# Optimization experiments

Hardware: AMD Instinct MI355X
Metric: run time of the kernel (lower is better)

The kernel has to match this reference:

```python
import jax, jax.numpy as jnp
import numpy as np

C64 = jnp.complex64


def _rx(theta):
    # RX(t) = [[cos(t/2), -i sin(t/2)], [-i sin(t/2), cos(t/2)]]; theta scalar or [B]
    h = 0.5 * theta
    c = jnp.cos(h).astype(C64)
    s = (-1j * jnp.sin(h)).astype(C64)
    return jnp.stack([jnp.stack([c, s], -1), jnp.stack([s, c], -1)], -2)


def _ry(theta):
    h = 0.5 * theta
    c = jnp.cos(h).astype(C64)
    s = jnp.sin(h).astype(C64)
    return jnp.stack([jnp.stack([c, -s], -1), jnp.stack([s, c], -1)], -2)


def _rz(theta):
    h = 0.5 * theta
    em = jnp.exp(-1j * h).astype(C64)
    ep = jnp.exp(1j * h).astype(C64)
    z = jnp.zeros_like(em)
    return jnp.stack([jnp.stack([em, z], -1), jnp.stack([z, ep], -1)], -2)


def _apply_1q(state, U, q):
    # state: [B, 2^Q] complex; wire 0 is the most significant bit.
    B = state.shape[0]
    s = state.reshape(B, 2 ** q, 2, -1)
    if U.ndim == 3:  # batched gate [B,2,2]
        s = jnp.einsum('bij,bajc->baic', U, s)
    else:  # shared gate [2,2]
        s = jnp.einsum('ij,bajc->baic', U, s)
    return s.reshape(B, -1)


def _cnot_adj(state, q):
    # CNOT with control q, target q+1 (adjacent wires)
    B = state.shape[0]
    s = state.reshape(B, 2 ** q, 2, 2, -1)
    s = s.at[:, :, 1].set(s[:, :, 1, ::-1])
    return s.reshape(B, -1)


def _pqc(context, W, b, pqc_params):
    Q = W.shape[0]
    L = pqc_params.shape[0]
    angles = jnp.pi * jnp.tanh(context @ W.T + b)  # [B, Q]
    B = angles.shape[0]
    state = jnp.zeros((B, 2 ** Q), C64).at[:, 0].set(1.0)
    # data-encoding RX layer (batch-dependent angles)
    for q in range(Q):
        state = _apply_1q(state, _rx(angles[:, q]), q)
    # variational layers
    for l in range(L):
        for q in range(Q):
            state = _apply_1q(state, _rx(pqc_params[l, q, 0]), q)
            state = _apply_1q(state, _ry(pqc_params[l, q, 1]), q)
            state = _apply_1q(state, _rz(pqc_params[l, q, 2]), q)
        for q in range(Q - 1):
            state = _cnot_adj(state, q)
    # <Z_q> expectation for every wire
    probs = state.real ** 2 + state.imag ** 2  # [B, 2^Q]
    p = probs.reshape((B,) + (2,) * Q)
    z = [p.sum(tuple(i + 1 for i in range(Q) if i != q)) for q in range(Q)]  # each [B,2]
    z = jnp.stack(z, -1)  # [B, 2, Q] -> wait: stack of [B,2] on -1 -> [B,2,Q]
    return z[:, 0, :] - z[:, 1, :]  # [B, Q]


def setup_inputs() -> dict:
    key = jax.random.key(0)
    k0, k1, k2, k3 = jax.random.split(key, 4)
    B, D, Q, L = 512, 256, 16, 4
    context = jax.random.normal(k0, (B, D), jnp.float32)
    W = jax.random.normal(k1, (Q, D), jnp.float32) / np.float32(np.sqrt(D))
    b = 0.01 * jax.random.normal(k2, (Q,), jnp.float32)
    pqc_params = 0.01 * jax.random.normal(k3, (L, Q, 3), jnp.float32)
    return {"context": context, "W": W, "b": b, "pqc_params": pqc_params}


def reference(context, W, b, pqc_params):
    return _pqc(context, W, b, pqc_params)
```

## Files before the change

kernel.cpp:

```cpp
#include <hip/hip_runtime.h>
#include <math.h>

#define NQ   16
#define NTH  256
#define NB   512

typedef float2 c32;

__device__ __forceinline__ c32 cmul(c32 a, c32 b) {
    return make_float2(a.x*b.x - a.y*b.y, a.x*b.y + a.y*b.x);
}
__device__ __forceinline__ c32 cfma_(c32 a, c32 b, c32 acc) {
    acc.x = fmaf(a.x, b.x, fmaf(-a.y, b.y, acc.x));
    acc.y = fmaf(a.x, b.y, fmaf( a.y, b.x, acc.y));
    return acc;
}
__device__ __forceinline__ c32 cfmaConjA(c32 a, c32 b, c32 acc) {
    acc.x = fmaf(a.x, b.x, fmaf( a.y, b.y, acc.x));
    acc.y = fmaf(a.x, b.y, fmaf(-a.y, b.x, acc.y));
    return acc;
}
__device__ __forceinline__ c32 cmulConjA(c32 a, c32 b) {
    return cfmaConjA(a, b, make_float2(0.f, 0.f));
}
__device__ __forceinline__ c32 cadd(c32 a, c32 b){ return make_float2(a.x+b.x, a.y+b.y); }


__global__ __launch_bounds__(NTH, 2)
void pqc_mps_kernel(const float* __restrict__ ctx,
                    const float* __restrict__ Wm,
                    const float* __restrict__ bias,
                    const float* __restrict__ params,
                    float* __restrict__ out)
{
    __shared__ c32 Ac[14][272];
    __shared__ c32 A0c[16];
    __shared__ c32 A15v[32];
    __shared__ c32 Renv[15][144];
    __shared__ c32 Ssto[15][144];
    __shared__ c32 TR[272];
    __shared__ c32 TL[272];
    __shared__ c32 Lbuf[144];
    __shared__ c32 Ug[256];
    __shared__ c32 wv[64];
    __shared__ float angles[NQ];

    const int b = blockIdx.x;
    const int t = threadIdx.x;

    {
        const int q = t >> 4, g = t & 15;
        const float* crow = ctx + b * 256;
        const float* wrow = Wm + q * 256;
        float s = 0.f;
        #pragma unroll
        for (int j = 0; j < 16; ++j)
            s += crow[g + 16*j] * wrow[g + 16*j];
        #pragma unroll
        for (int m = 8; m; m >>= 1) s += __shfl_xor(s, m);
        if (g == 0) angles[q] = 3.14159265358979323846f * tanhf(s + bias[q]);
    }
    if (t < 64) {
        const float a  = params[t*3 + 0];
        const float bb = params[t*3 + 1];
        const float c  = params[t*3 + 2];
        const float ha = 0.5f*a, hb = 0.5f*bb, hc = 0.5f*c;
        const float ca = cosf(ha), sa = sinf(ha);
        const float cb = cosf(hb), sb = sinf(hb);
        const float cz = cosf(hc), sz = sinf(hc);
        const c32 m00 = make_float2( cb*ca,  sb*sa);
        const c32 m01 = make_float2(-sb*ca, -cb*sa);
        const c32 m10 = make_float2( sb*ca, -cb*sa);
        const c32 m11 = make_float2( cb*ca, -sb*sa);
        const c32 e0 = make_float2(cz, -sz);
        const c32 e1 = make_float2(cz,  sz);
        Ug[t*4 + 0] = cmul(e0, m00);
        Ug[t*4 + 1] = cmul(e0, m01);
        Ug[t*4 + 2] = cmul(e1, m10);
        Ug[t*4 + 3] = cmul(e1, m11);
    }
    __syncthreads();

    if (t < 64) {
        const int q = t >> 2, k = (t>>1)&1, i = t&1;
        const float h = 0.5f * angles[q];
        const float ch = cosf(h), sh = sinf(h);
        const int r0 = (i ^ k) << 1;
        const c32 u0 = Ug[(q<<2) + r0];
        const c32 u1 = Ug[(q<<2) + r0 + 1];
        wv[t] = make_float2(u0.x*ch + u1.y*sh, u0.y*ch - u1.x*sh);
    }
    __syncthreads();

    {
        const int r = t & 7, i = (t>>3)&1, a = t>>4;
        const int m0 = r&1, m1 = (r>>1)&1, m2 = r>>2;
        const int k0 = a&1, k1 = (a>>1)&1, k2 = (a>>2)&1, k3 = a>>3;
        #pragma unroll
        for (int q = 1; q <= 14; ++q) {
            const c32 u3 = Ug[((48+q)<<2) + ((i ^k3)<<1) + m2];
            const c32 u2 = Ug[((32+q)<<2) + ((m2^k2)<<1) + m1];
            const c32 u1 = Ug[((16+q)<<2) + ((m1^k1)<<1) + m0];
            const c32 ww = wv[(q<<2) + (k0<<1) + m0];
            Ac[q-1][a*17 + i*8 + r] = cmul(cmul(u3, u2), cmul(u1, ww));
        }
        if (t < 16) {
            const c32 u3 = Ug[(48<<2) + (i <<1) + m2];
            const c32 u2 = Ug[(32<<2) + (m2<<1) + m1];
            const c32 u1 = Ug[(16<<2) + (m1<<1) + m0];
            A0c[t] = cmul(cmul(u3, u2), cmul(u1, wv[m0]));
        }
        if (t >= 64 && t < 96) {
            const int idx = t - 64, aa = idx >> 1, ii = idx & 1;
            const int K0 = aa&1, K1 = (aa>>1)&1, K2 = (aa>>2)&1, K3 = aa>>3;
            c32 y1[2], y2[2];
            #pragma unroll
            for (int j1 = 0; j1 < 2; ++j1) {
                const int rr = (j1 ^ K1) << 1;
                y1[j1] = cfma_(Ug[((16+15)<<2)+rr], wv[60 + (K0<<1)],
                         cmul (Ug[((16+15)<<2)+rr+1], wv[60 + (K0<<1) + 1]));
            }
            #pragma unroll
            for (int j2 = 0; j2 < 2; ++j2) {
                const int rr = (j2 ^ K2) << 1;
                y2[j2] = cfma_(Ug[((32+15)<<2)+rr], y1[0],
                         cmul (Ug[((32+15)<<2)+rr+1], y1[1]));
            }
            const int rr = (ii ^ K3) << 1;
            A15v[(aa<<1)+ii] = cfma_(Ug[((48+15)<<2)+rr], y2[0],
                               cmul (Ug[((48+15)<<2)+rr+1], y2[1]));
        }
    }
    __syncthreads();

    if (t < 128) {
        const int m = t>>6, bl = (t>>3)&7, bp = t&7;
        c32 acc = cmulConjA(A15v[((m<<3)+bl)<<1],       A15v[((m<<3)+bp)<<1]);
        acc     = cfmaConjA(A15v[(((m<<3)+bl)<<1) + 1], A15v[(((m<<3)+bp)<<1) + 1], acc);
        Renv[14][m*72 + bl*9 + bp] = acc;
    } else {
        const int u = t-128, i = u>>6, bl = (u>>3)&7, bp = u&7;
        const c32 s = cmulConjA(A0c[(i<<3)+bl], A0c[(i<<3)+bp]);
        Ssto[0][i*72 + bl*9 + bp] = s;
        Lbuf   [i*72 + bl*9 + bp] = s;
    }
    __syncthreads();

    for (int s = 1; s <= 14; ++s) {
        const c32* Ap = Ac[14 - s];
        const c32* Rn = Renv[15 - s];
        const c32* As = Ac[s - 1];

        {
            const int bb = t>>4, i = (t>>3)&1, gp = t&7;
            const int m = bb>>3, al = bb&7;
            c32 tr = make_float2(0.f,0.f), tl = make_float2(0.f,0.f);
            #pragma unroll
            for (int g = 0; g < 8; ++g) {
                tr = cfmaConjA(Ap[bb*17 + i*8 + g], Rn[i*72 + g*9 + gp], tr);
                tl = cfma_(Lbuf[m*72 + al*9 + g], As[(m*8+g)*17 + i*8 + gp], tl);
            }
            TR[bb*17 + i*8 + gp] = tr;
            TL[bb*17 + i*8 + gp] = tl;
        }
        __syncthreads();

        if (t < 128) {
            const int m = t>>6, bl = (t>>3)&7, bp = t&7;
            const c32* trow = &TR[(m*8+bl)*17];
            const c32* arow = &Ap[(m*8+bp)*17];
            c32 r0 = make_float2(0.f,0.f), r1 = make_float2(0.f,0.f);
            #pragma unroll
            for (int ig = 0; ig < 16; ig += 2) {
                r0 = cfma_(trow[ig],   arow[ig],   r0);
                r1 = cfma_(trow[ig+1], arow[ig+1], r1);
            }
            Renv[14-s][m*72 + bl*9 + bp] = cadd(r0, r1);
        } else {
            const int u = t-128, i = u>>6, bl = (u>>3)&7, bp = u&7;
            c32 s0 = make_float2(0.f,0.f), s1 = make_float2(0.f,0.f);
            #pragma unroll
            for (int a = 0; a < 16; a += 2) {
                s0 = cfmaConjA(As[ a   *17 + i*8 + bl], TL[ a   *17 + i*8 + bp], s0);
                s1 = cfmaConjA(As[(a+1)*17 + i*8 + bl], TL[(a+1)*17 + i*8 + bp], s1);
            }
            const c32 sv = cadd(s0, s1);
            Ssto[s][i*72 + bl*9 + bp] = sv;
            Lbuf   [i*72 + bl*9 + bp] = sv;
        }
        __syncthreads();
    }

    {
        const int q = t >> 4, g = t & 15;
        float val = 0.f;
        if (q < 15) {
            const int i = g>>3, bl = g&7;
            const float sign = i ? -1.f : 1.f;
            const c32* Sq = &Ssto[q][i*72 + bl*9];
            const c32* Rq = &Renv[q][i*72 + bl*9];
            #pragma unroll
            for (int j = 0; j < 8; ++j)
                val += sign * (Sq[j].x*Rq[j].x - Sq[j].y*Rq[j].y);
        } else {
            const int m = g>>3, al = g&7;
            const c32 a0 = A15v[((m*8+al)<<1) + 0];
            const c32 a1 = A15v[((m*8+al)<<1) + 1];
            #pragma unroll
            for (int j = 0; j < 8; ++j) {
                c32 d = cmulConjA(a0, A15v[((m*8+j)<<1) + 0]);
                const c32 d1 = cmulConjA(a1, A15v[((m*8+j)<<1) + 1]);
                d.x -= d1.x; d.y -= d1.y;
                const c32 Lv = Lbuf[m*72 + al*9 + j];
                val += Lv.x*d.x - Lv.y*d.y;
            }
        }
        #pragma unroll
        for (int mm = 8; mm; mm >>= 1) val += __shfl_xor(val, mm);
        if (g == 0) out[b*NQ + q] = val;
    }
}

extern "C" void kernel_launch(void* const* d_in, const int* in_sizes, int n_in,
                              void* d_out, int out_size, void* d_ws, size_t ws_size,
                              hipStream_t stream) {
    const float* ctx    = (const float*)d_in[0];
    const float* Wm     = (const float*)d_in[1];
    const float* bias   = (const float*)d_in[2];
    const float* params = (const float*)d_in[3];
    float* out = (float*)d_out;
    (void)in_sizes; (void)n_in; (void)out_size; (void)d_ws; (void)ws_size;
    pqc_mps_kernel<<<NB, NTH, 0, stream>>>(ctx, Wm, bias, params, out);
}
```

Baseline: 79.42 us.

## Split MPS environment sweeps into independent wavefronts with Hermitian-symmetric outputs

The block shrinks to 128 threads. The right-environment sweep runs on wavefront 0 and the left-environment sweep on wavefront 1, each independently, which removes the per-step block-wide __syncthreads barriers. Each thread computes a 2x2 register tile of the intermediate contraction. Only the upper triangle of the Hermitian environment matrices is computed, and the conjugate is mirrored into the other half. The angle dot product now uses float4 loads. The cost is less parallelism per block and a reliance on wavefront-synchronous execution within each 64-lane wave for the shared-memory handoffs between sub-steps.

New measurement: 78.95 us. About the same (-0.6%).

```diff
diff --git a/kernel.cpp b/kernel.cpp
--- a/kernel.cpp
+++ b/kernel.cpp
@@ -2,8 +2,9 @@
 #include <math.h>
 
 #define NQ   16
-#define NTH  256
 #define NB   512
+#define NTH  128
+#define PI_F 3.14159265358979323846f
 
 typedef float2 c32;
 
@@ -23,23 +24,24 @@
 __device__ __forceinline__ c32 cmulConjA(c32 a, c32 b) {
     return cfmaConjA(a, b, make_float2(0.f, 0.f));
 }
+__device__ __forceinline__ c32 conjc(c32 a){ return make_float2(a.x, -a.y); }
 __device__ __forceinline__ c32 cadd(c32 a, c32 b){ return make_float2(a.x+b.x, a.y+b.y); }
 
 
-__global__ __launch_bounds__(NTH, 2)
+__global__ __launch_bounds__(NTH)
 void pqc_mps_kernel(const float* __restrict__ ctx,
                     const float* __restrict__ Wm,
                     const float* __restrict__ bias,
                     const float* __restrict__ params,
                     float* __restrict__ out)
 {
-    __shared__ c32 Ac[14][272];
+    __shared__ c32 Ac[14*272];
     __shared__ c32 A0c[16];
     __shared__ c32 A15v[32];
-    __shared__ c32 Renv[15][144];
-    __shared__ c32 Ssto[15][144];
-    __shared__ c32 TR[272];
-    __shared__ c32 TL[272];
+    __shared__ c32 Renv[15*144];
+    __shared__ c32 Ssto[15*144];
+    __shared__ c32 TRb[272];
+    __shared__ c32 TLT[272];
     __shared__ c32 Lbuf[144];
     __shared__ c32 Ug[256];
     __shared__ c32 wv[64];
@@ -47,18 +49,20 @@
 
     const int b = blockIdx.x;
     const int t = threadIdx.x;
+    const int lane = t & 63;
 
     {
-        const int q = t >> 4, g = t & 15;
-        const float* crow = ctx + b * 256;
-        const float* wrow = Wm + q * 256;
+        const int q = t >> 3, g = t & 7;
+        const float4* c4 = (const float4*)(ctx + (size_t)b * 256);
+        const float4* w4 = (const float4*)(Wm  + (size_t)q * 256);
         float s = 0.f;
         #pragma unroll
-        for (int j = 0; j < 16; ++j)
-            s += crow[g + 16*j] * wrow[g + 16*j];
-        #pragma unroll
-        for (int m = 8; m; m >>= 1) s += __shfl_xor(s, m);
-        if (g == 0) angles[q] = 3.14159265358979323846f * tanhf(s + bias[q]);
+        for (int j = 0; j < 8; ++j) {
+            const float4 x = c4[g + 8*j], y = w4[g + 8*j];
+            s = fmaf(x.x,y.x, fmaf(x.y,y.y, fmaf(x.z,y.z, fmaf(x.w,y.w, s))));
+        }
+        s += __shfl_xor(s, 4); s += __shfl_xor(s, 2); s += __shfl_xor(s, 1);
+        if (g == 0) angles[q] = PI_F * tanhf(s + bias[q]);
     }
     if (t < 64) {
         const float a  = params[t*3 + 0];
@@ -93,18 +97,23 @@
     __syncthreads();
 
     {
-        const int r = t & 7, i = (t>>3)&1, a = t>>4;
-        const int m0 = r&1, m1 = (r>>1)&1, m2 = r>>2;
-        const int k0 = a&1, k1 = (a>>1)&1, k2 = (a>>2)&1, k3 = a>>3;
-        #pragma unroll
         for (int q = 1; q <= 14; ++q) {
-            const c32 u3 = Ug[((48+q)<<2) + ((i ^k3)<<1) + m2];
-            const c32 u2 = Ug[((32+q)<<2) + ((m2^k2)<<1) + m1];
-            const c32 u1 = Ug[((16+q)<<2) + ((m1^k1)<<1) + m0];
-            const c32 ww = wv[(q<<2) + (k0<<1) + m0];
-            Ac[q-1][a*17 + i*8 + r] = cmul(cmul(u3, u2), cmul(u1, ww));
+            #pragma unroll
+            for (int h = 0; h < 2; ++h) {
+                const int idx = t + 128*h;
+                const int r = idx & 7, i = (idx>>3)&1, a = idx>>4;
+                const int m0 = r&1, m1 = (r>>1)&1, m2 = r>>2;
+                const int k0 = a&1, k1 = (a>>1)&1, k2 = (a>>2)&1, k3 = a>>3;
+                const c32 u3 = Ug[((48+q)<<2) + ((i ^k3)<<1) + m2];
+                const c32 u2 = Ug[((32+q)<<2) + ((m2^k2)<<1) + m1];
+                const c32 u1 = Ug[((16+q)<<2) + ((m1^k1)<<1) + m0];
+                const c32 ww = wv[(q<<2) + (k0<<1) + m0];
+                Ac[(q-1)*272 + a*17 + i*8 + r] = cmul(cmul(u3, u2), cmul(u1, ww));
+            }
         }
         if (t < 16) {
+            const int i = t>>3, r = t&7;
+            const int m0 = r&1, m1 = (r>>1)&1, m2 = r>>2;
             const c32 u3 = Ug[(48<<2) + (i <<1) + m2];
             const c32 u2 = Ug[(32<<2) + (m2<<1) + m1];
             const c32 u1 = Ug[(16<<2) + (m1<<1) + m0];
@@ -133,91 +142,201 @@
     }
     __syncthreads();
 
-    if (t < 128) {
-        const int m = t>>6, bl = (t>>3)&7, bp = t&7;
-        c32 acc = cmulConjA(A15v[((m<<3)+bl)<<1],       A15v[((m<<3)+bp)<<1]);
-        acc     = cfmaConjA(A15v[(((m<<3)+bl)<<1) + 1], A15v[(((m<<3)+bp)<<1) + 1], acc);
-        Renv[14][m*72 + bl*9 + bp] = acc;
+    int blJ = 0, bpJ, mJ;
+    {
+        const int r = (lane < 36) ? lane : lane - 36;
+        mJ = (lane >= 36) ? 1 : 0;
+        while ((blJ+1)*(blJ+2)/2 <= r) ++blJ;
+        bpJ = r - blJ*(blJ+1)/2;
+    }
+    const bool has2 = (lane < 8);
+
+    if (t < 64) {
+        const int bbp = lane>>3, iS = (lane>>2)&1, gpp = lane&3;
+        const int bb0 = 2*bbp, bb1 = bb0+1, gq0 = 2*gpp, gq1 = gq0+1;
+
+        {
+            c32 acc = make_float2(0.f,0.f);
+            #pragma unroll
+            for (int i = 0; i < 2; ++i)
+                acc = cfmaConjA(A15v[(mJ*8+blJ)*2+i], A15v[(mJ*8+bpJ)*2+i], acc);
+            Renv[14*144 + mJ*72 + blJ*9 + bpJ] = acc;
+            if (blJ != bpJ) Renv[14*144 + mJ*72 + bpJ*9 + blJ] = conjc(acc);
+            if (has2) {
+                c32 a2 = make_float2(0.f,0.f);
+                #pragma unroll
+                for (int i = 0; i < 2; ++i)
+                    a2 = cfmaConjA(A15v[(8+7)*2+i], A15v[(8+lane)*2+i], a2);
+                Renv[14*144 + 72 + 7*9 + lane] = a2;
+                if (lane != 7) Renv[14*144 + 72 + lane*9 + 7] = conjc(a2);
+            }
+        }
+        for (int s = 1; s <= 14; ++s) {
+            const c32* Ap = Ac + (14-s)*272;
+            const c32* Rn = Renv + (15-s)*144;
+            c32*       Ro = Renv + (14-s)*144;
+            c32 aA[8], aB[8], rA[8], rB[8];
+            #pragma unroll
+            for (int g = 0; g < 8; ++g) {
+                aA[g] = Ap[bb0*17 + iS*8 + g];
+                aB[g] = Ap[bb1*17 + iS*8 + g];
+                rA[g] = Rn[iS*72 + gq0*9 + g];
+                rB[g] = Rn[iS*72 + gq1*9 + g];
+            }
+            c32 t00=make_float2(0.f,0.f), t01=t00, t10=t00, t11=t00;
+            #pragma unroll
+            for (int g = 0; g < 8; ++g) {
+                t00 = cfma_(aA[g], rA[g], t00); t01 = cfma_(aA[g], rB[g], t01);
+                t10 = cfma_(aB[g], rA[g], t10); t11 = cfma_(aB[g], rB[g], t11);
+            }
+            TRb[bb0*17 + iS*8 + gq0] = conjc(t00);
+            TRb[bb0*17 + iS*8 + gq1] = conjc(t01);
+            TRb[bb1*17 + iS*8 + gq0] = conjc(t10);
+            TRb[bb1*17 + iS*8 + gq1] = conjc(t11);
+            {
+                const c32* tr = TRb + (mJ*8+blJ)*17;
+                const c32* ap = Ap  + (mJ*8+bpJ)*17;
+                c32 r0 = make_float2(0.f,0.f), r1 = r0;
+                #pragma unroll
+                for (int k = 0; k < 16; k += 2) {
+                    r0 = cfma_(tr[k],   ap[k],   r0);
+                    r1 = cfma_(tr[k+1], ap[k+1], r1);
+                }
+                const c32 acc = cadd(r0, r1);
+                Ro[mJ*72 + blJ*9 + bpJ] = acc;
+                if (blJ != bpJ) Ro[mJ*72 + bpJ*9 + blJ] = conjc(acc);
+            }
+            if (has2) {
+                const c32* tr = TRb + (8+7)*17;
+                const c32* ap = Ap  + (8+lane)*17;
+                c32 r0 = make_float2(0.f,0.f), r1 = r0;
+                #pragma unroll
+                for (int k = 0; k < 16; k += 2) {
+                    r0 = cfma_(tr[k],   ap[k],   r0);
+                    r1 = cfma_(tr[k+1], ap[k+1], r1);
+                }
+                const c32 acc = cadd(r0, r1);
+                Ro[72 + 7*9 + lane] = acc;
+                if (lane != 7) Ro[72 + lane*9 + 7] = conjc(acc);
+            }
+        }
     } else {
-        const int u = t-128, i = u>>6, bl = (u>>3)&7, bp = u&7;
-        const c32 s = cmulConjA(A0c[(i<<3)+bl], A0c[(i<<3)+bp]);
-        Ssto[0][i*72 + bl*9 + bp] = s;
-        Lbuf   [i*72 + bl*9 + bp] = s;
+        const int ap_ = lane>>3, iS = (lane>>2)&1, bpp = lane&3;
+        const int a0_ = 2*ap_, a1_ = a0_+1, bq0 = 2*bpp, bq1 = bq0+1;
+        const int mS = ap_>>2, al0 = a0_&7, al1 = a1_&7;
+
+        {
+            const c32 sv = cmulConjA(A0c[mJ*8+blJ], A0c[mJ*8+bpJ]);
+            Ssto[mJ*72 + blJ*9 + bpJ] = sv;
+            Lbuf[mJ*72 + blJ*9 + bpJ] = sv;
+            if (blJ != bpJ) {
+                const c32 cs = conjc(sv);
+                Ssto[mJ*72 + bpJ*9 + blJ] = cs;
+                Lbuf[mJ*72 + bpJ*9 + blJ] = cs;
+            }
+            if (has2) {
+                const c32 s2 = cmulConjA(A0c[8+7], A0c[8+lane]);
+                Ssto[72 + 7*9 + lane] = s2;
+                Lbuf[72 + 7*9 + lane] = s2;
+                if (lane != 7) {
+                    const c32 cs = conjc(s2);
+                    Ssto[72 + lane*9 + 7] = cs;
+                    Lbuf[72 + lane*9 + 7] = cs;
+                }
+            }
+        }
+        for (int s = 1; s <= 14; ++s) {
+            const c32* As = Ac + (s-1)*272;
+            c32*       So = Ssto + s*144;
+            c32 lA[8], lB[8], c0v[8], c1v[8];
+            #pragma unroll
+            for (int g = 0; g < 8; ++g) {
+                lA[g]  = Lbuf[mS*72 + al0*9 + g];
+                lB[g]  = Lbuf[mS*72 + al1*9 + g];
+                c0v[g] = As[(mS*8+g)*17 + iS*8 + bq0];
+                c1v[g] = As[(mS*8+g)*17 + iS*8 + bq1];
+            }
+            c32 t00=make_float2(0.f,0.f), t01=t00, t10=t00, t11=t00;
+            #pragma unroll
+            for (int g = 0; g < 8; ++g) {
+                t00 = cfma_(lA[g], c0v[g], t00); t01 = cfma_(lA[g], c1v[g], t01);
+                t10 = cfma_(lB[g], c0v[g], t10); t11 = cfma_(lB[g], c1v[g], t11);
+            }
+            TLT[(iS*8 + bq0)*17 + a0_] = t00;
+            TLT[(iS*8 + bq1)*17 + a0_] = t01;
+            TLT[(iS*8 + bq0)*17 + a1_] = t10;
+            TLT[(iS*8 + bq1)*17 + a1_] = t11;
+            {
+                const c32* tl = TLT + (mJ*8+bpJ)*17;
+                c32 s0 = make_float2(0.f,0.f), s1 = s0;
+                #pragma unroll
+                for (int k = 0; k < 16; k += 2) {
+                    s0 = cfmaConjA(As[ k   *17 + mJ*8 + blJ], tl[k],   s0);
+                    s1 = cfmaConjA(As[(k+1)*17 + mJ*8 + blJ], tl[k+1], s1);
+                }
+                const c32 acc = cadd(s0, s1);
+                So[mJ*72 + blJ*9 + bpJ] = acc;
+                Lbuf[mJ*72 + blJ*9 + bpJ] = acc;
+                if (blJ != bpJ) {
+                    const c32 cs = conjc(acc);
+                    So[mJ*72 + bpJ*9 + blJ] = cs;
+                    Lbuf[mJ*72 + bpJ*9 + blJ] = cs;
+                }
+            }
+            if (has2) {
+                const c32* tl = TLT + (8+lane)*17;
+                c32 s0 = make_float2(0.f,0.f), s1 = s0;
+                #pragma unroll
+                for (int k = 0; k < 16; k += 2) {
+                    s0 = cfmaConjA(As[ k   *17 + 8 + 7], tl[k],   s0);
+                    s1 = cfmaConjA(As[(k+1)*17 + 8 + 7], tl[k+1], s1);
+                }
+                const c32 acc = cadd(s0, s1);
+                So[72 + 7*9 + lane] = acc;
+                Lbuf[72 + 7*9 + lane] = acc;
+                if (lane != 7) {
+                    const c32 cs = conjc(acc);
+                    So[72 + lane*9 + 7] = cs;
+                    Lbuf[72 + lane*9 + 7] = cs;
+                }
+            }
+        }
     }
     __syncthreads();
 
-    for (int s = 1; s <= 14; ++s) {
-        const c32* Ap = Ac[14 - s];
-        const c32* Rn = Renv[15 - s];
-        const c32* As = Ac[s - 1];
-
-        {
-            const int bb = t>>4, i = (t>>3)&1, gp = t&7;
-            const int m = bb>>3, al = bb&7;
-            c32 tr = make_float2(0.f,0.f), tl = make_float2(0.f,0.f);
-            #pragma unroll
-            for (int g = 0; g < 8; ++g) {
-                tr = cfmaConjA(Ap[bb*17 + i*8 + g], Rn[i*72 + g*9 + gp], tr);
-                tl = cfma_(Lbuf[m*72 + al*9 + g], As[(m*8+g)*17 + i*8 + gp], tl);
-            }
-            TR[bb*17 + i*8 + gp] = tr;
-            TL[bb*17 + i*8 + gp] = tl;
-        }
-        __syncthreads();
-
-        if (t < 128) {
-            const int m = t>>6, bl = (t>>3)&7, bp = t&7;
-            const c32* trow = &TR[(m*8+bl)*17];
-            const c32* arow = &Ap[(m*8+bp)*17];
-            c32 r0 = make_float2(0.f,0.f), r1 = make_float2(0.f,0.f);
-            #pragma unroll
-            for (int ig = 0; ig < 16; ig += 2) {
-                r0 = cfma_(trow[ig],   arow[ig],   r0);
-                r1 = cfma_(trow[ig+1], arow[ig+1], r1);
-            }
-            Renv[14-s][m*72 + bl*9 + bp] = cadd(r0, r1);
-        } else {
-            const int u = t-128, i = u>>6, bl = (u>>3)&7, bp = u&7;
-            c32 s0 = make_float2(0.f,0.f), s1 = make_float2(0.f,0.f);
-            #pragma unroll
-            for (int a = 0; a < 16; a += 2) {
-                s0 = cfmaConjA(As[ a   *17 + i*8 + bl], TL[ a   *17 + i*8 + bp], s0);
-                s1 = cfmaConjA(As[(a+1)*17 + i*8 + bl], TL[(a+1)*17 + i*8 + bp], s1);
-            }
-            const c32 sv = cadd(s0, s1);
-            Ssto[s][i*72 + bl*9 + bp] = sv;
-            Lbuf   [i*72 + bl*9 + bp] = sv;
-        }
-        __syncthreads();
-    }
-
     {
-        const int q = t >> 4, g = t & 15;
-        float val = 0.f;
-        if (q < 15) {
-            const int i = g>>3, bl = g&7;
-            const float sign = i ? -1.f : 1.f;
-            const c32* Sq = &Ssto[q][i*72 + bl*9];
-            const c32* Rq = &Renv[q][i*72 + bl*9];
-            #pragma unroll
-            for (int j = 0; j < 8; ++j)
-                val += sign * (Sq[j].x*Rq[j].x - Sq[j].y*Rq[j].y);
-        } else {
-            const int m = g>>3, al = g&7;
-            const c32 a0 = A15v[((m*8+al)<<1) + 0];
-            const c32 a1 = A15v[((m*8+al)<<1) + 1];
-            #pragma unroll
-            for (int j = 0; j < 8; ++j) {
-                c32 d = cmulConjA(a0, A15v[((m*8+j)<<1) + 0]);
-                const c32 d1 = cmulConjA(a1, A15v[((m*8+j)<<1) + 1]);
-                d.x -= d1.x; d.y -= d1.y;
-                const c32 Lv = Lbuf[m*72 + al*9 + j];
-                val += Lv.x*d.x - Lv.y*d.y;
-            }
-        }
+        const int g = t & 15, qb = t >> 4;
         #pragma unroll
-        for (int mm = 8; mm; mm >>= 1) val += __shfl_xor(val, mm);
-        if (g == 0) out[b*NQ + q] = val;
+        for (int h = 0; h < 2; ++h) {
+            const int qq = qb + 8*h;
+            float val = 0.f;
+            if (qq < 15) {
+                const int i = g>>3, blz = g&7;
+                const float sign = i ? -1.f : 1.f;
+                const c32* Sq = Ssto + qq*144 + i*72 + blz*9;
+                const c32* Rq = Renv + qq*144 + i*72 + blz*9;
+                #pragma unroll
+                for (int j = 0; j < 8; ++j)
+                    val += sign * (Sq[j].x*Rq[j].x - Sq[j].y*Rq[j].y);
+            } else {
+                const int m = g>>3, al = g&7;
+                const c32 a0 = A15v[((m*8+al)<<1) + 0];
+                const c32 a1 = A15v[((m*8+al)<<1) + 1];
+                #pragma unroll
+                for (int j = 0; j < 8; ++j) {
+                    c32 d = cmulConjA(a0, A15v[((m*8+j)<<1) + 0]);
+                    const c32 d1 = cmulConjA(a1, A15v[((m*8+j)<<1) + 1]);
+                    d.x -= d1.x; d.y -= d1.y;
+                    const c32 Lv = Lbuf[m*72 + al*9 + j];
+                    val += Lv.x*d.x - Lv.y*d.y;
+                }
+            }
+            val += __shfl_xor(val, 8);
+            val += __shfl_xor(val, 4);
+            val += __shfl_xor(val, 2);
+            val += __shfl_xor(val, 1);
+            if (g == 0) out[b*NQ + qq] = val;
+        }
     }
 }
 
```
